# Performance work log

Hardware: AMD Instinct MI355X
Metric: run time of the kernel (lower is better)

The kernel has to match this reference:

```python
import jax, jax.numpy as jnp
import numpy as np

SIZE = 20
DIM = 2 ** SIZE
BATCH = 16
INV_SQRT2 = 1.0 / np.sqrt(2.0).astype(np.float32)

# spec[x] = sum_i (1 - 2*bit_i(x)) for homogeneous z-field (z = ones, zz = {})
_idx = np.arange(DIM, dtype=np.int64)
_popcount = np.zeros(DIM, dtype=np.int64)
for _k in range(SIZE):
    _popcount += (_idx >> _k) & 1
SPEC = jnp.asarray((SIZE - 2 * _popcount).astype(np.float32))  # [DIM]


def _hadamard_all(xr, xi):
    # Apply H on every qubit site sequentially (same math as the gather+sign
    # loop in GateHadamard, expressed as the standard butterfly):
    # for bit=0 slot: (a + b)/sqrt2 ; for bit=1 slot: (a - b)/sqrt2
    B = xr.shape[0]
    for site in range(SIZE):
        lo = 2 ** site
        hi = 2 ** (SIZE - 1 - site)
        xr4 = xr.reshape(B, lo, 2, hi)
        xi4 = xi.reshape(B, lo, 2, hi)
        ar, br = xr4[:, :, 0], xr4[:, :, 1]
        ai, bi = xi4[:, :, 0], xi4[:, :, 1]
        xr = (jnp.stack([ar + br, ar - br], axis=2) * INV_SQRT2).reshape(B, DIM)
        xi = (jnp.stack([ai + bi, ai - bi], axis=2) * INV_SQRT2).reshape(B, DIM)
    return xr, xi


def setup_inputs() -> dict:
    key = jax.random.key(0)
    k1, k2 = jax.random.split(key)
    x_real = jax.random.normal(k1, (BATCH, DIM), dtype=jnp.float32)
    x_imag = jax.random.normal(k2, (BATCH, DIM), dtype=jnp.float32)
    t = jnp.ones((1,), dtype=jnp.float32)
    return {"x_real": x_real, "x_imag": x_imag, "t": t}


def reference(x_real, x_imag, t):
    xr, xi = _hadamard_all(x_real, x_imag)
    # phase multiply: (cos(sp) - i sin(sp)) * (xr + i xi)
    sp = t[0] * SPEC  # [DIM]
    c, s = jnp.cos(sp), jnp.sin(sp)
    yr = c * xr + s * xi
    yi = c * xi - s * xr
    xr, xi = _hadamard_all(yr, yi)
    return jnp.stack([xr, xi])  # [2, BATCH, DIM] (real, imag)
```

## Files before the change

kernel.cpp:

```cpp
#include <hip/hip_runtime.h>
#include <hip/hip_fp16.h>
#include <math.h>

#define DIMN (1 << 20)

typedef unsigned int uint2v __attribute__((ext_vector_type(2)));

__device__ __forceinline__ unsigned int h2u(__half2 v){ union{__half2 h; unsigned int u;} x; x.h=v; return x.u; }
__device__ __forceinline__ __half2 u2h(unsigned int v){ union{unsigned int u; __half2 h;} x; x.u=v; return x.h; }

__device__ __forceinline__ void bf(float& a, float& b) { float s = a + b; b = a - b; a = s; }

template<int CTRL>
__device__ __forceinline__ float dppf(float x) {
    return __int_as_float(__builtin_amdgcn_mov_dpp(__float_as_int(x), CTRL, 0xF, 0xF, true));
}
template<int CTRL>
__device__ __forceinline__ unsigned int dppu(unsigned int x) {
    return (unsigned int)__builtin_amdgcn_mov_dpp((int)x, CTRL, 0xF, 0xF, true);
}
__device__ __forceinline__ float xor4_f(float x) { return dppf<0x1B>(dppf<0x141>(x)); }
__device__ __forceinline__ unsigned int xor4_u(unsigned int x) { return dppu<0x1B>(dppu<0x141>(x)); }

__device__ __forceinline__ float bfly16_f(float x, float sgn) {
#if __has_builtin(__builtin_amdgcn_permlane16_swap)
    uint2v r = __builtin_amdgcn_permlane16_swap(__float_as_uint(x), __float_as_uint(x), false, false);
    return fmaf(sgn, __uint_as_float(r.y), __uint_as_float(r.x));
#else
    float p = __shfl_xor(x, 16);
    return fmaf(sgn, x, p);
#endif
}
__device__ __forceinline__ float bfly32_f(float x, float sgn) {
#if __has_builtin(__builtin_amdgcn_permlane32_swap)
    uint2v r = __builtin_amdgcn_permlane32_swap(__float_as_uint(x), __float_as_uint(x), false, false);
    return fmaf(sgn, __uint_as_float(r.y), __uint_as_float(r.x));
#else
    float p = __shfl_xor(x, 32);
    return fmaf(sgn, x, p);
#endif
}
__device__ __forceinline__ __half2 bfly16_h2(__half2 x, __half2 sgn) {
#if __has_builtin(__builtin_amdgcn_permlane16_swap)
    uint2v r = __builtin_amdgcn_permlane16_swap(h2u(x), h2u(x), false, false);
    return __hfma2(u2h(r.y), sgn, u2h(r.x));
#else
    __half2 p = u2h((unsigned)__shfl_xor((int)h2u(x), 16));
    return __hfma2(x, sgn, p);
#endif
}
__device__ __forceinline__ __half2 bfly32_h2(__half2 x, __half2 sgn) {
#if __has_builtin(__builtin_amdgcn_permlane32_swap)
    uint2v r = __builtin_amdgcn_permlane32_swap(h2u(x), h2u(x), false, false);
    return __hfma2(u2h(r.y), sgn, u2h(r.x));
#else
    __half2 p = u2h((unsigned)__shfl_xor((int)h2u(x), 32));
    return __hfma2(x, sgn, p);
#endif
}

__device__ __forceinline__ void wht16_f32(float v[16], int lane) {
    #pragma unroll
    for (int s = 1; s < 16; s <<= 1)
        #pragma unroll
        for (int r = 0; r < 16; r++)
            if (!(r & s)) bf(v[r], v[r ^ s]);
    {   float sgn = (lane & 1) ? -1.0f : 1.0f;
        #pragma unroll
        for (int r = 0; r < 16; r++) { float p = dppf<0xB1>(v[r]); v[r] = fmaf(sgn, v[r], p); } }
    {   float sgn = (lane & 2) ? -1.0f : 1.0f;
        #pragma unroll
        for (int r = 0; r < 16; r++) { float p = dppf<0x4E>(v[r]); v[r] = fmaf(sgn, v[r], p); } }
    {   float sgn = (lane & 4) ? -1.0f : 1.0f;
        #pragma unroll
        for (int r = 0; r < 16; r++) { float p = xor4_f(v[r]); v[r] = fmaf(sgn, v[r], p); } }
    {   float sgn = (lane & 8) ? -1.0f : 1.0f;
        #pragma unroll
        for (int r = 0; r < 16; r++) { float p = dppf<0x128>(v[r]); v[r] = fmaf(sgn, v[r], p); } }
    {   float sgn = (lane & 16) ? -1.0f : 1.0f;
        #pragma unroll
        for (int r = 0; r < 16; r++) v[r] = bfly16_f(v[r], sgn); }
    {   float sgn = (lane & 32) ? -1.0f : 1.0f;
        #pragma unroll
        for (int r = 0; r < 16; r++) v[r] = bfly32_f(v[r], sgn); }
}

__device__ __forceinline__ void wht16_h2(__half2 v[16], int lane) {
    #pragma unroll
    for (int s = 1; s < 16; s <<= 1)
        #pragma unroll
        for (int r = 0; r < 16; r++)
            if (!(r & s)) {
                __half2 t = __hadd2(v[r], v[r ^ s]);
                v[r ^ s]  = __hsub2(v[r], v[r ^ s]);
                v[r] = t;
            }
    {   __half2 sgn = __float2half2_rn((lane & 1) ? -1.0f : 1.0f);
        #pragma unroll
        for (int r = 0; r < 16; r++) { __half2 p = u2h(dppu<0xB1>(h2u(v[r]))); v[r] = __hfma2(v[r], sgn, p); } }
    {   __half2 sgn = __float2half2_rn((lane & 2) ? -1.0f : 1.0f);
        #pragma unroll
        for (int r = 0; r < 16; r++) { __half2 p = u2h(dppu<0x4E>(h2u(v[r]))); v[r] = __hfma2(v[r], sgn, p); } }
    {   __half2 sgn = __float2half2_rn((lane & 4) ? -1.0f : 1.0f);
        #pragma unroll
        for (int r = 0; r < 16; r++) { __half2 p = u2h(xor4_u(h2u(v[r]))); v[r] = __hfma2(v[r], sgn, p); } }
    {   __half2 sgn = __float2half2_rn((lane & 8) ? -1.0f : 1.0f);
        #pragma unroll
        for (int r = 0; r < 16; r++) { __half2 p = u2h(dppu<0x128>(h2u(v[r]))); v[r] = __hfma2(v[r], sgn, p); } }
    {   __half2 sgn = __float2half2_rn((lane & 16) ? -1.0f : 1.0f);
        #pragma unroll
        for (int r = 0; r < 16; r++) v[r] = bfly16_h2(v[r], sgn); }
    {   __half2 sgn = __float2half2_rn((lane & 32) ? -1.0f : 1.0f);
        #pragma unroll
        for (int r = 0; r < 16; r++) v[r] = bfly32_h2(v[r], sgn); }
}

__device__ __forceinline__ void xorperm4(unsigned int a[4], int m) {
    bool s0 = (m & 1) != 0, s1 = (m & 2) != 0;
    unsigned int t0 = s0 ? a[1] : a[0], t1 = s0 ? a[0] : a[1];
    unsigned int t2 = s0 ? a[3] : a[2], t3 = s0 ? a[2] : a[3];
    a[0] = s1 ? t2 : t0; a[1] = s1 ? t3 : t1;
    a[2] = s1 ? t0 : t2; a[3] = s1 ? t1 : t3;
}

__device__ __forceinline__ void xorperm8(unsigned int a[8], int m) {
    bool s0 = (m & 1) != 0, s1 = (m & 2) != 0, s2 = (m & 4) != 0;
    unsigned int b0 = s0 ? a[1] : a[0], b1 = s0 ? a[0] : a[1];
    unsigned int b2 = s0 ? a[3] : a[2], b3 = s0 ? a[2] : a[3];
    unsigned int b4 = s0 ? a[5] : a[4], b5 = s0 ? a[4] : a[5];
    unsigned int b6 = s0 ? a[7] : a[6], b7 = s0 ? a[6] : a[7];
    unsigned int c0 = s1 ? b2 : b0, c1 = s1 ? b3 : b1;
    unsigned int c2 = s1 ? b0 : b2, c3 = s1 ? b1 : b3;
    unsigned int c4 = s1 ? b6 : b4, c5 = s1 ? b7 : b5;
    unsigned int c6 = s1 ? b4 : b6, c7 = s1 ? b5 : b7;
    a[0] = s2 ? c4 : c0; a[1] = s2 ? c5 : c1;
    a[2] = s2 ? c6 : c2; a[3] = s2 ? c7 : c3;
    a[4] = s2 ? c0 : c4; a[5] = s2 ? c1 : c5;
    a[6] = s2 ? c2 : c6; a[7] = s2 ? c3 : c7;
}

__global__ __launch_bounds__(256, 4) void pA_kernel(const float* __restrict__ xr,
                                                    const float* __restrict__ xi,
                                                    __half2* __restrict__ ws,
                                                    const float* __restrict__ tptr) {
    const int tid = threadIdx.x, lane = tid & 63, w = tid >> 6;
    const int rt = blockIdx.x * 4 + w;
    const float tval = tptr[0];
    const int pcl = __popc(lane);
    float cs[5], sn[5];
    #pragma unroll
    for (int k = 0; k < 5; k++) {
        float ang = tval * (float)(10 - 2 * (pcl + k));
        float s, c;
        __sincosf(ang, &s, &c);
        cs[k] = c * 0.03125f;
        sn[k] = s * 0.03125f;
    }
    const float* re = xr + (size_t)rt * 1024;
    const float* im = xi + (size_t)rt * 1024;
    float vr[16], vi[16];
    #pragma unroll
    for (int q = 0; q < 2; q++) {
        const int base = q * 512 + lane * 8;
        float4 a0 = *(const float4*)(re + base);
        float4 a1 = *(const float4*)(re + base + 4);
        float4 b0 = *(const float4*)(im + base);
        float4 b1 = *(const float4*)(im + base + 4);
        vr[q*8+0]=a0.x*0.03125f; vr[q*8+1]=a0.y*0.03125f; vr[q*8+2]=a0.z*0.03125f; vr[q*8+3]=a0.w*0.03125f;
        vr[q*8+4]=a1.x*0.03125f; vr[q*8+5]=a1.y*0.03125f; vr[q*8+6]=a1.z*0.03125f; vr[q*8+7]=a1.w*0.03125f;
        vi[q*8+0]=b0.x*0.03125f; vi[q*8+1]=b0.y*0.03125f; vi[q*8+2]=b0.z*0.03125f; vi[q*8+3]=b0.w*0.03125f;
        vi[q*8+4]=b1.x*0.03125f; vi[q*8+5]=b1.y*0.03125f; vi[q*8+6]=b1.z*0.03125f; vi[q*8+7]=b1.w*0.03125f;
    }
    wht16_f32(vr, lane);
    wht16_f32(vi, lane);
    #pragma unroll
    for (int r = 0; r < 16; r++) {
        const int pr = __popc(r);
        float x = vr[r], y = vi[r];
        vr[r] = fmaf(cs[pr], x,  sn[pr] * y);
        vi[r] = fmaf(cs[pr], y, -sn[pr] * x);
    }
    wht16_f32(vr, lane);
    wht16_f32(vi, lane);
    __half2* wp = ws + (size_t)rt * 1024;
    #pragma unroll
    for (int q = 0; q < 2; q++) {
        const int base = q * 512 + lane * 8;
        uint4 u0, u1;
        u0.x = h2u(__floats2half2_rn(vr[q*8+0], vi[q*8+0]));
        u0.y = h2u(__floats2half2_rn(vr[q*8+1], vi[q*8+1]));
        u0.z = h2u(__floats2half2_rn(vr[q*8+2], vi[q*8+2]));
        u0.w = h2u(__floats2half2_rn(vr[q*8+3], vi[q*8+3]));
        u1.x = h2u(__floats2half2_rn(vr[q*8+4], vi[q*8+4]));
        u1.y = h2u(__floats2half2_rn(vr[q*8+5], vi[q*8+5]));
        u1.z = h2u(__floats2half2_rn(vr[q*8+6], vi[q*8+6]));
        u1.w = h2u(__floats2half2_rn(vr[q*8+7], vi[q*8+7]));
        *(uint4*)(wp + base)     = u0;
        *(uint4*)(wp + base + 4) = u1;
    }
}

__global__ __launch_bounds__(512, 4) void pB_kernel(const __half2* __restrict__ ws,
                                                    float* __restrict__ out,
                                                    const float* __restrict__ tptr) {
    __shared__ unsigned int tile[1024][16];
    const int tid = threadIdx.x, lane = tid & 63, w = tid >> 6;

    int wg  = blockIdx.x;
    int swz = (wg & 7) * 128 + (wg >> 3);
    const int b  = swz >> 6;
    const int g  = swz & 63;
    const int c0 = g * 16;
    const float tval = tptr[0];

    const int pcl = __popc(lane);
    __half2 c2k[5], s2k[5];
    #pragma unroll
    for (int k = 0; k < 5; k++) {
        float ang = tval * (float)(10 - 2 * (pcl + k));
        float s, c;
        __sincosf(ang, &s, &c);
        c2k[k] = __float2half2_rn(c * 0.03125f);
        s2k[k] = __halves2half2(__float2half(s * 0.03125f),
                                __float2half(-s * 0.03125f));
    }

    const __half2* src = ws + (size_t)b * DIMN + c0;

    #pragma unroll
    for (int it = 0; it < 8; it++) {
        int f = it * 512 + tid;
        int h = f >> 2, qd = f & 3;
        uint4 a = *(const uint4*)(src + (size_t)h * 1024 + qd * 4);
        unsigned int g4[4] = {a.x, a.y, a.z, a.w};
        int e = (h >> 2) & 15;
        xorperm4(g4, e & 3);
        int dq = qd ^ (e >> 2);
        *(uint4*)&tile[h][dq * 4] = make_uint4(g4[0], g4[1], g4[2], g4[3]);
    }
    __syncthreads();

    const int e4 = (lane >> 2) & 15;
    const int cp0 = w ^ e4;
    const __half2 sc = __float2half2_rn(0.03125f);
    __half2 v0[16], v1[16];
    #pragma unroll
    for (int r = 0; r < 16; r++) {
        v0[r] = __hmul2(u2h(tile[r * 64 + lane][cp0]),     sc);
        v1[r] = __hmul2(u2h(tile[r * 64 + lane][cp0 ^ 8]), sc);
    }

    wht16_h2(v0, lane);
    wht16_h2(v1, lane);

    #pragma unroll
    for (int r = 0; r < 16; r++) {
        const int pr = __popc(r);
        unsigned int u0 = h2u(v0[r]), u1 = h2u(v1[r]);
        __half2 vs0 = u2h((u0 >> 16) | (u0 << 16));
        __half2 vs1 = u2h((u1 >> 16) | (u1 << 16));
        v0[r] = __hfma2(c2k[pr], v0[r], __hmul2(s2k[pr], vs0));
        v1[r] = __hfma2(c2k[pr], v1[r], __hmul2(s2k[pr], vs1));
    }

    wht16_h2(v0, lane);
    wht16_h2(v1, lane);

    #pragma unroll
    for (int r = 0; r < 16; r++) {
        tile[r * 64 + lane][cp0]     = h2u(v0[r]);
        tile[r * 64 + lane][cp0 ^ 8] = h2u(v1[r]);
    }
    __syncthreads();

    float* outR = out + (size_t)b * DIMN + c0;
    float* outI = out + (size_t)16 * DIMN + (size_t)b * DIMN + c0;
    #pragma unroll
    for (int it = 0; it < 4; it++) {
        int f = it * 512 + tid;
        int h = f >> 1, q8 = f & 1;
        int e = (h >> 2) & 15;
        int base = (q8 ^ (e >> 3)) * 8;
        uint4 u0 = *(const uint4*)&tile[h][base];
        uint4 u1 = *(const uint4*)&tile[h][base + 4];
        unsigned int w8[8] = {u0.x, u0.y, u0.z, u0.w, u1.x, u1.y, u1.z, u1.w};
        xorperm8(w8, e & 7);
        float4 r0, r1, i0, i1;
        r0.x = __low2float(u2h(w8[0])); i0.x = __high2float(u2h(w8[0]));
        r0.y = __low2float(u2h(w8[1])); i0.y = __high2float(u2h(w8[1]));
        r0.z = __low2float(u2h(w8[2])); i0.z = __high2float(u2h(w8[2]));
        r0.w = __low2float(u2h(w8[3])); i0.w = __high2float(u2h(w8[3]));
        r1.x = __low2float(u2h(w8[4])); i1.x = __high2float(u2h(w8[4]));
        r1.y = __low2float(u2h(w8[5])); i1.y = __high2float(u2h(w8[5]));
        r1.z = __low2float(u2h(w8[6])); i1.z = __high2float(u2h(w8[6]));
        r1.w = __low2float(u2h(w8[7])); i1.w = __high2float(u2h(w8[7]));
        size_t off = (size_t)h * 1024 + q8 * 8;
        *(float4*)(outR + off)     = r0;
        *(float4*)(outR + off + 4) = r1;
        *(float4*)(outI + off)     = i0;
        *(float4*)(outI + off + 4) = i1;
    }
}

__device__ __forceinline__ void wht10_f4(float4 v[4], int lane) {
    #pragma unroll
    for (int r = 0; r < 4; r++) {
        bf(v[r].x, v[r].y); bf(v[r].z, v[r].w);
        bf(v[r].x, v[r].z); bf(v[r].y, v[r].w);
    }
    #pragma unroll
    for (int m = 1; m <= 32; m <<= 1) {
        float sgn = (lane & m) ? -1.0f : 1.0f;
        #pragma unroll
        for (int r = 0; r < 4; r++) {
            float px = __shfl_xor(v[r].x, m), py = __shfl_xor(v[r].y, m);
            float pz = __shfl_xor(v[r].z, m), pw = __shfl_xor(v[r].w, m);
            v[r].x = fmaf(sgn, v[r].x, px); v[r].y = fmaf(sgn, v[r].y, py);
            v[r].z = fmaf(sgn, v[r].z, pz); v[r].w = fmaf(sgn, v[r].w, pw);
        }
    }
    bf(v[0].x, v[1].x); bf(v[0].y, v[1].y); bf(v[0].z, v[1].z); bf(v[0].w, v[1].w);
    bf(v[2].x, v[3].x); bf(v[2].y, v[3].y); bf(v[2].z, v[3].z); bf(v[2].w, v[3].w);
    bf(v[0].x, v[2].x); bf(v[0].y, v[2].y); bf(v[0].z, v[2].z); bf(v[0].w, v[2].w);
    bf(v[1].x, v[3].x); bf(v[1].y, v[3].y); bf(v[1].z, v[3].z); bf(v[1].w, v[3].w);
}

__global__ __launch_bounds__(256) void pass13_kernel(const float* __restrict__ srcA,
                                                     const float* __restrict__ srcB,
                                                     float* __restrict__ dst) {
    const int tid = threadIdx.x, lane = tid & 63, w = tid >> 6;
    const int rt0 = blockIdx.x * 16 + w * 4;
    const float* src = (rt0 < 16384) ? (srcA + (size_t)rt0 * 1024)
                                     : (srcB + (size_t)(rt0 - 16384) * 1024);
    float* d = dst + (size_t)rt0 * 1024;
    float4 v[4][4];
    #pragma unroll
    for (int rr = 0; rr < 4; rr++)
        #pragma unroll
        for (int r = 0; r < 4; r++)
            v[rr][r] = *(const float4*)(src + rr * 1024 + r * 256 + lane * 4);
    #pragma unroll
    for (int rr = 0; rr < 4; rr++) {
        wht10_f4(v[rr], lane);
        #pragma unroll
        for (int r = 0; r < 4; r++) {
            float4 o;
            o.x = v[rr][r].x * 0.03125f; o.y = v[rr][r].y * 0.03125f;
            o.z = v[rr][r].z * 0.03125f; o.w = v[rr][r].w * 0.03125f;
            *(float4*)(d + rr * 1024 + r * 256 + lane * 4) = o;
        }
    }
}

__global__ __launch_bounds__(256) void pass2f_kernel(float* __restrict__ out,
                                                     const float* __restrict__ tptr) {
    __shared__ __align__(16) float tile[2][1024][8];
    const int tid = threadIdx.x, lane = tid & 63, w = tid >> 6;
    int wg = blockIdx.x;
    int swz = (wg & 7) * 256 + (wg >> 3);
    const int b = swz >> 7, g = swz & 127;
    const int c0 = g * 8;
    const float tval = tptr[0];
    float* baseR = out + (size_t)b * DIMN;
    float* baseI = out + (size_t)16 * DIMN + (size_t)b * DIMN;
    float4 tmp[2][8];
    #pragma unroll
    for (int comp = 0; comp < 2; comp++) {
        const float* src = comp ? baseI : baseR;
        #pragma unroll
        for (int it = 0; it < 8; it++) {
            int f4id = it * 256 + tid;
            int h = f4id >> 1, q = f4id & 1;
            tmp[comp][it] = *(const float4*)(src + (size_t)h * 1024 + c0 + q * 4);
        }
    }
    #pragma unroll
    for (int comp = 0; comp < 2; comp++) {
        #pragma unroll
        for (int it = 0; it < 8; it++) {
            int f4id = it * 256 + tid;
            int h = f4id >> 1, q = f4id & 1;
            int e = (h >> 2) & 7, elo = e & 3;
            float4 val = tmp[comp][it];
            bool s0 = (elo & 1) != 0;
            float x1 = s0 ? val.y : val.x, y1 = s0 ? val.x : val.y;
            float z1 = s0 ? val.w : val.z, w1 = s0 ? val.z : val.w;
            bool s1 = (elo & 2) != 0;
            float x2 = s1 ? z1 : x1, y2 = s1 ? w1 : y1;
            float z2 = s1 ? x1 : z1, w2 = s1 ? y1 : w1;
            int qp = q ^ (e >> 2);
            *(float4*)&tile[comp][h][qp * 4] = make_float4(x2, y2, z2, w2);
        }
    }
    __syncthreads();
    float vr[2][16], vi[2][16];
    #pragma unroll
    for (int r = 0; r < 16; r++) {
        int h = r * 64 + lane;
        int e = (lane >> 2) & 7;
        #pragma unroll
        for (int cc = 0; cc < 2; cc++) {
            int cp = (2 * w + cc) ^ e;
            vr[cc][r] = tile[0][h][cp];
            vi[cc][r] = tile[1][h][cp];
        }
    }
    const int pcl = __popc(lane);
    #pragma unroll
    for (int cc = 0; cc < 2; cc++) {
        wht16_f32(vr[cc], lane);
        wht16_f32(vi[cc], lane);
        const int cg = c0 + 2 * w + cc;
        const int pbase = pcl + __popc(cg);
        float csk[5], snk[5];
        #pragma unroll
        for (int k = 0; k < 5; k++) {
            float ang = tval * (float)(20 - 2 * (pbase + k));
            __sincosf(ang, &snk[k], &csk[k]);
        }
        #pragma unroll
        for (int r = 0; r < 16; r++) {
            const int pr = __popc(r);
            float cv = csk[pr], sv = snk[pr];
            float xr = vr[cc][r] * 0.03125f, xi = vi[cc][r] * 0.03125f;
            vr[cc][r] = fmaf(cv, xr, sv * xi);
            vi[cc][r] = fmaf(cv, xi, -sv * xr);
        }
        wht16_f32(vr[cc], lane);
        wht16_f32(vi[cc], lane);
    }
    #pragma unroll
    for (int r = 0; r < 16; r++) {
        int h = r * 64 + lane;
        int e = (lane >> 2) & 7;
        #pragma unroll
        for (int cc = 0; cc < 2; cc++) {
            int cp = (2 * w + cc) ^ e;
            tile[0][h][cp] = vr[cc][r] * 0.03125f;
            tile[1][h][cp] = vi[cc][r] * 0.03125f;
        }
    }
    __syncthreads();
    #pragma unroll
    for (int comp = 0; comp < 2; comp++) {
        float* dstg = comp ? baseI : baseR;
        #pragma unroll
        for (int it = 0; it < 8; it++) {
            int f4id = it * 256 + tid;
            int h = f4id >> 1, q = f4id & 1;
            int e = (h >> 2) & 7, elo = e & 3;
            int qp = q ^ (e >> 2);
            float4 sv = *(const float4*)&tile[comp][h][qp * 4];
            bool s0 = (elo & 1) != 0;
            float x1 = s0 ? sv.y : sv.x, y1 = s0 ? sv.x : sv.y;
            float z1 = s0 ? sv.w : sv.z, w1 = s0 ? sv.z : sv.w;
            bool s1 = (elo & 2) != 0;
            float x2 = s1 ? z1 : x1, y2 = s1 ? w1 : y1;
            float z2 = s1 ? x1 : z1, w2 = s1 ? y1 : w1;
            *(float4*)(dstg + (size_t)h * 1024 + c0 + q * 4) = make_float4(x2, y2, z2, w2);
        }
    }
}

extern "C" void kernel_launch(void* const* d_in, const int* in_sizes, int n_in,
                              void* d_out, int out_size, void* d_ws, size_t ws_size,
                              hipStream_t stream) {
    const float* xr = (const float*)d_in[0];
    const float* xi = (const float*)d_in[1];
    const float* t  = (const float*)d_in[2];
    float* out = (float*)d_out;

    const size_t need = (size_t)16 * DIMN * sizeof(__half2);
    if (ws_size >= need) {
        __half2* ws = (__half2*)d_ws;
        pA_kernel<<<4096, 256, 0, stream>>>(xr, xi, ws, t);
        pB_kernel<<<1024, 512, 0, stream>>>(ws, out, t);
    } else {
        pass13_kernel<<<2048, 256, 0, stream>>>(xr, xi, out);
        pass2f_kernel<<<2048, 256, 0, stream>>>(out, t);
        pass13_kernel<<<2048, 256, 0, stream>>>(out, out + (size_t)16 * DIMN, out);
    }
}
```

Before: 97.21 us.

## Widen pB tile to 32 columns with 1024-thread blocks

The second-pass kernel now processes 32 columns per workgroup instead of 16, using 1024 threads and a 128 KB LDS tile, with a redesigned XOR swizzle for the transpose and store phases. Each row's global reads and writes become 128-byte contiguous segments per block rather than 64, which is meant to improve memory coalescing and DRAM efficiency. The cost is twice the LDS per block, which limits how many blocks can be resident per CU, plus larger barriers across 16 waves.

```diff
diff --git a/kernel.cpp b/kernel.cpp
--- a/kernel.cpp
+++ b/kernel.cpp
@@ -200,17 +200,17 @@
     }
 }
 
-__global__ __launch_bounds__(512, 4) void pB_kernel(const __half2* __restrict__ ws,
-                                                    float* __restrict__ out,
-                                                    const float* __restrict__ tptr) {
-    __shared__ unsigned int tile[1024][16];
+__global__ __launch_bounds__(1024, 4) void pB_kernel(const __half2* __restrict__ ws,
+                                                     float* __restrict__ out,
+                                                     const float* __restrict__ tptr) {
+    __shared__ unsigned int tile[1024][32];
     const int tid = threadIdx.x, lane = tid & 63, w = tid >> 6;
 
     int wg  = blockIdx.x;
-    int swz = (wg & 7) * 128 + (wg >> 3);
-    const int b  = swz >> 6;
-    const int g  = swz & 63;
-    const int c0 = g * 16;
+    int swz = (wg & 7) * 64 + (wg >> 3);
+    const int b  = swz >> 5;
+    const int g  = swz & 31;
+    const int c0 = g * 32;
     const float tval = tptr[0];
 
     const int pcl = __popc(lane);
@@ -229,25 +229,25 @@
 
     #pragma unroll
     for (int it = 0; it < 8; it++) {
-        int f = it * 512 + tid;
-        int h = f >> 2, qd = f & 3;
+        int f = it * 1024 + tid;
+        int h = f >> 3, qd = f & 7;
         uint4 a = *(const uint4*)(src + (size_t)h * 1024 + qd * 4);
         unsigned int g4[4] = {a.x, a.y, a.z, a.w};
-        int e = (h >> 2) & 15;
+        int e = h & 31;
         xorperm4(g4, e & 3);
         int dq = qd ^ (e >> 2);
         *(uint4*)&tile[h][dq * 4] = make_uint4(g4[0], g4[1], g4[2], g4[3]);
     }
     __syncthreads();
 
-    const int e4 = (lane >> 2) & 15;
-    const int cp0 = w ^ e4;
+    const int el = lane & 31;
+    const int cp0 = w ^ el;
     const __half2 sc = __float2half2_rn(0.03125f);
     __half2 v0[16], v1[16];
     #pragma unroll
     for (int r = 0; r < 16; r++) {
-        v0[r] = __hmul2(u2h(tile[r * 64 + lane][cp0]),     sc);
-        v1[r] = __hmul2(u2h(tile[r * 64 + lane][cp0 ^ 8]), sc);
+        v0[r] = __hmul2(u2h(tile[r * 64 + lane][cp0]),      sc);
+        v1[r] = __hmul2(u2h(tile[r * 64 + lane][cp0 ^ 16]), sc);
     }
 
     wht16_h2(v0, lane);
@@ -268,8 +268,8 @@
 
     #pragma unroll
     for (int r = 0; r < 16; r++) {
-        tile[r * 64 + lane][cp0]     = h2u(v0[r]);
-        tile[r * 64 + lane][cp0 ^ 8] = h2u(v1[r]);
+        tile[r * 64 + lane][cp0]      = h2u(v0[r]);
+        tile[r * 64 + lane][cp0 ^ 16] = h2u(v1[r]);
     }
     __syncthreads();
 
@@ -277,23 +277,27 @@
     float* outI = out + (size_t)16 * DIMN + (size_t)b * DIMN + c0;
     #pragma unroll
     for (int it = 0; it < 4; it++) {
-        int f = it * 512 + tid;
-        int h = f >> 1, q8 = f & 1;
-        int e = (h >> 2) & 15;
-        int base = (q8 ^ (e >> 3)) * 8;
-        uint4 u0 = *(const uint4*)&tile[h][base];
-        uint4 u1 = *(const uint4*)&tile[h][base + 4];
-        unsigned int w8[8] = {u0.x, u0.y, u0.z, u0.w, u1.x, u1.y, u1.z, u1.w};
-        xorperm8(w8, e & 7);
+        int f = it * 1024 + tid;
+        int h = f >> 2, q8 = f & 3;
+        int e = h & 31;
+        int m = e & 3, eh = e >> 2;
+        int dq0 = (2 * q8)     ^ eh;
+        int dq1 = (2 * q8 + 1) ^ eh;
+        uint4 A = *(const uint4*)&tile[h][dq0 * 4];
+        uint4 B = *(const uint4*)&tile[h][dq1 * 4];
+        unsigned int a4[4] = {A.x, A.y, A.z, A.w};
+        unsigned int b4[4] = {B.x, B.y, B.z, B.w};
+        xorperm4(a4, m);
+        xorperm4(b4, m);
         float4 r0, r1, i0, i1;
-        r0.x = __low2float(u2h(w8[0])); i0.x = __high2float(u2h(w8[0]));
-        r0.y = __low2float(u2h(w8[1])); i0.y = __high2float(u2h(w8[1]));
-        r0.z = __low2float(u2h(w8[2])); i0.z = __high2float(u2h(w8[2]));
-        r0.w = __low2float(u2h(w8[3])); i0.w = __high2float(u2h(w8[3]));
-        r1.x = __low2float(u2h(w8[4])); i1.x = __high2float(u2h(w8[4]));
-        r1.y = __low2float(u2h(w8[5])); i1.y = __high2float(u2h(w8[5]));
-        r1.z = __low2float(u2h(w8[6])); i1.z = __high2float(u2h(w8[6]));
-        r1.w = __low2float(u2h(w8[7])); i1.w = __high2float(u2h(w8[7]));
+        r0.x = __low2float(u2h(a4[0])); i0.x = __high2float(u2h(a4[0]));
+        r0.y = __low2float(u2h(a4[1])); i0.y = __high2float(u2h(a4[1]));
+        r0.z = __low2float(u2h(a4[2])); i0.z = __high2float(u2h(a4[2]));
+        r0.w = __low2float(u2h(a4[3])); i0.w = __high2float(u2h(a4[3]));
+        r1.x = __low2float(u2h(b4[0])); i1.x = __high2float(u2h(b4[0]));
+        r1.y = __low2float(u2h(b4[1])); i1.y = __high2float(u2h(b4[1]));
+        r1.z = __low2float(u2h(b4[2])); i1.z = __high2float(u2h(b4[2]));
+        r1.w = __low2float(u2h(b4[3])); i1.w = __high2float(u2h(b4[3]));
         size_t off = (size_t)h * 1024 + q8 * 8;
         *(float4*)(outR + off)     = r0;
         *(float4*)(outR + off + 4) = r1;
@@ -474,7 +478,7 @@
     if (ws_size >= need) {
         __half2* ws = (__half2*)d_ws;
         pA_kernel<<<4096, 256, 0, stream>>>(xr, xi, ws, t);
-        pB_kernel<<<1024, 512, 0, stream>>>(ws, out, t);
+        pB_kernel<<<512, 1024, 0, stream>>>(ws, out, t);
     } else {
         pass13_kernel<<<2048, 256, 0, stream>>>(xr, xi, out);
         pass2f_kernel<<<2048, 256, 0, stream>>>(out, t);
```

New measurement: 112.1 us. 1.15x slower.
